# Optimization experiments

Hardware: AMD Instinct MI355X
Metric: run time of the kernel (lower is better)

## Reference

```python
import jax, jax.numpy as jnp
import numpy as np

RATIO, NH, NG, KS, RF, UP = 4, 2, 2, 3, 11.0, 2


def _cln(t, g, b):
    # channel-wise LayerNorm on NCHW (LayerNormProxy), eps=1e-5
    mu = t.mean(axis=1, keepdims=True)
    var = ((t - mu) ** 2).mean(axis=1, keepdims=True)
    return (t - mu) * jax.lax.rsqrt(var + 1e-5) * g[None, :, None, None] + b[None, :, None, None]


def _resize_ac(img, oH, oW):
    # bilinear resize, align_corners=True (F.interpolate)
    H, W = img.shape[-2], img.shape[-1]
    ys = jnp.arange(oH, dtype=img.dtype) * ((H - 1) / (oH - 1))
    y0 = jnp.clip(jnp.floor(ys), 0, H - 2).astype(jnp.int32)
    wy = ys - y0.astype(img.dtype)
    xs = jnp.arange(oW, dtype=img.dtype) * ((W - 1) / (oW - 1))
    x0 = jnp.clip(jnp.floor(xs), 0, W - 2).astype(jnp.int32)
    wx = xs - x0.astype(img.dtype)
    t = img[..., y0, :] * (1.0 - wy)[:, None] + img[..., y0 + 1, :] * wy[:, None]
    return t[..., x0] * (1.0 - wx) + t[..., x0 + 1] * wx


def _grid_sample(img, iy, ix):
    # bilinear grid_sample, padding_mode='zeros', align_corners=True
    # img [Bg,Cx,H,W]; iy,ix [Bg,N] unnormalized input-pixel coords
    H, W = img.shape[-2], img.shape[-1]
    def one(im, yy, xx):
        y0f, x0f = jnp.floor(yy), jnp.floor(xx)
        wy, wx = yy - y0f, xx - x0f
        y0, x0 = y0f.astype(jnp.int32), x0f.astype(jnp.int32)
        def gat(yi, xi):
            valid = ((yi >= 0) & (yi < H) & (xi >= 0) & (xi < W)).astype(im.dtype)
            return im[:, jnp.clip(yi, 0, H - 1), jnp.clip(xi, 0, W - 1)] * valid[None]
        return (gat(y0, x0) * ((1 - wy) * (1 - wx))[None]
                + gat(y0, x0 + 1) * ((1 - wy) * wx)[None]
                + gat(y0 + 1, x0) * (wy * (1 - wx))[None]
                + gat(y0 + 1, x0 + 1) * (wy * wx)[None])
    return jax.vmap(one)(img, iy, ix)


def _conv2d(x, w, groups=1):
    return jax.lax.conv_general_dilated(x, w, (1, 1), 'SAME', feature_group_count=groups,
                                        dimension_numbers=('NCHW', 'OIHW', 'NCHW'))


def _forward(x, ln_g, ln_b, Wq, Wk, dw_w, off_ln_g, off_ln_b, off_w, off_b, rpb):
    B, C, H, W = x.shape
    hidden = C // RATIO
    gc = hidden // NG
    c2 = hidden // NH          # attn_dim per head
    oH, oW = int(H * UP), int(W * UP)
    N1, n = oH * oW, KS * KS
    scale = c2 ** -0.5
    v = x
    xn = _cln(x, ln_g, ln_b)
    q = jnp.einsum('oc,bchw->bohw', Wq, xn)
    k = jnp.einsum('oc,bchw->bohw', Wk, xn)
    q = _resize_ac(q, oH, oW)                        # [B,hidden,oH,oW]
    # offset prediction
    q_off = q.reshape(B * NG, gc, oH, oW)
    t = _conv2d(q_off, dw_w, groups=gc)
    t = _cln(t, off_ln_g, off_ln_b)
    t = jax.nn.gelu(t, approximate=False)
    pred = _conv2d(t, off_w) + off_b[None, :, None, None]  # [Bg,2*ks^2,oH,oW]
    pad = (KS - 1) // 2
    rng = jnp.arange(-pad, pad + 1, dtype=x.dtype)
    base = jnp.stack(jnp.meshgrid(rng, rng, indexing='ij'), axis=-1)  # [KS,KS,2] (y,x)
    off = jnp.tanh(pred).reshape(B * NG, KS, KS, 2, oH, oW) * RF + base[None, :, :, :, None, None]
    py = off[:, :, :, 0] + jnp.arange(oH, dtype=x.dtype)[None, None, None, :, None]
    px = off[:, :, :, 1] + jnp.arange(oW, dtype=x.dtype)[None, None, None, None, :]
    # normalize over (oH-1,oW-1) then denormalize onto (H-1,W-1) input grid (align_corners)
    iy = (py * ((H - 1) / (oH - 1))).reshape(B * NG, -1)
    ix = (px * ((W - 1) / (oW - 1))).reshape(B * NG, -1)
    kg = k.reshape(B * NG, hidden // NG, H, W)
    vg = v.reshape(B * NG, C // NG, H, W)
    kf = _grid_sample(kg, iy, ix).reshape(B, NG, hidden // NG, n, oH, oW)
    vf = _grid_sample(vg, iy, ix).reshape(B, NG, C // NG, n, oH, oW)
    # -> [B, N1, n, g*c] -> [B, nh, N1, n, c]
    kf = kf.transpose(0, 4, 5, 3, 1, 2).reshape(B, N1, n, NH, hidden // NH).transpose(0, 3, 1, 2, 4)
    vf = vf.transpose(0, 4, 5, 3, 1, 2).reshape(B, N1, n, NH, C // NH).transpose(0, 3, 1, 2, 4)
    kf = kf + rpb                                     # relative position bias on K
    qh = q.reshape(B, NH, c2, N1).transpose(0, 1, 3, 2) * scale  # [B,nh,N1,c2]
    attn = jax.nn.softmax(jnp.einsum('bhnc,bhnkc->bhnk', qh, kf), axis=-1)
    out = jnp.einsum('bhnk,bhnkc->bhnc', attn, vf)    # [B,nh,N1,C/nh]
    return out.transpose(0, 1, 3, 2).reshape(B, C, oH, oW)


def setup_inputs() -> dict:
    key = jax.random.key(0)
    ks = jax.random.split(key, 8)
    B, C, H, W = 2, 256, 48, 48
    hidden = C // RATIO
    gc = hidden // NG
    c2 = hidden // NH
    f32 = jnp.float32
    return {
        'x': jax.random.normal(ks[0], (B, C, H, W), f32),
        'ln_g': jnp.ones((C,), f32),
        'ln_b': jnp.zeros((C,), f32),
        'Wq': jax.random.normal(ks[1], (hidden, C), f32) * 0.05,
        'Wk': jax.random.normal(ks[2], (hidden, C), f32) * 0.05,
        'dw_w': jax.random.normal(ks[3], (gc, 1, 3, 3), f32) * 0.1,
        'off_ln_g': jnp.ones((gc,), f32),
        'off_ln_b': jnp.zeros((gc,), f32),
        'off_w': jax.random.normal(ks[4], (2 * KS * KS, gc, 3, 3), f32) * 0.02,
        'off_b': jnp.zeros((2 * KS * KS,), f32),
        'rpb': jax.random.normal(ks[5], (1, NH, 1, KS * KS, c2), f32) * 0.02,
    }


def reference(x, ln_g, ln_b, Wq, Wk, dw_w, off_ln_g, off_ln_b, off_w, off_b, rpb):
    return _forward(x, ln_g, ln_b, Wq, Wk, dw_w, off_ln_g, off_ln_b, off_w, off_b, rpb)
```

## Files before the change

kernel.cpp:

```cpp
#include <hip/hip_runtime.h>
#include <hip/hip_fp16.h>
#include <cstdint>
#include <cmath>

#define NB 2
#define NC 256
#define HW 2304
#define HID 64
#define OH 96
#define OW 96
#define N1 9216
#define SCALE_ATTN 0.17677669529663689f
#define RESZ ((float)(47.0/95.0))

__device__ __host__ inline int ocb8(int w) { return w < 2 ? 3 * w : 6 + 2 * (w - 2); }
__device__ __host__ inline int cnt8(int w) { return w < 2 ? 3 : 2; }

__global__ void kA_prep(const float* __restrict__ x, const float* __restrict__ Wq,
                        const float* __restrict__ Wk, const float* __restrict__ off_w,
                        const float* __restrict__ dw_w, const float* __restrict__ off_b,
                        __half* __restrict__ v_nhwc, float* __restrict__ WT4,
                        float* __restrict__ dwT, float* __restrict__ wg2,
                        float* __restrict__ bsg2) {
    int blk = blockIdx.x;
    if (blk < 1152) {
        int pt = blk % 72;
        int t2 = blk / 72;
        int ct = t2 & 3;
        int bg = t2 >> 2;
        int b = bg >> 1, g = bg & 1;
        __shared__ float tile[32][33];
        int tx = threadIdx.x & 31, row = threadIdx.x >> 5;
#pragma unroll
        for (int r = 0; r < 4; r++) {
            int c = ct * 32 + row + r * 8;
            tile[row + r * 8][tx] = x[((size_t)(b * 256 + g * 128 + c)) * HW + pt * 32 + tx];
        }
        __syncthreads();
#pragma unroll
        for (int r = 0; r < 4; r++) {
            int p = pt * 32 + row + r * 8;
            v_nhwc[((size_t)bg * HW + p) * 128 + ct * 32 + tx] =
                __float2half(tile[tx][row + r * 8]);
        }
    } else {
        int idx = (blk - 1152) * 256 + threadIdx.x;
        if (idx < 32768) {
            int c = idx >> 7, t = idx & 127;
            float v = (t < 64) ? Wq[t * 256 + c] : Wk[(t - 64) * 256 + c];
            WT4[(((size_t)(c >> 2) * 128) + t) * 4 + (c & 3)] = v;
        } else if (idx < 32768 + 288) {
            int i = idx - 32768;
            int wi = i >> 5, c = i & 31;
            dwT[i] = dw_w[c * 9 + wi];
        } else if (idx < 32768 + 288 + 8 * 288 * 3) {
            int i = idx - (32768 + 288);
            int w = i / 864, r = i - w * 864;
            int kk = r / 3, j = r - kk * 3;
            wg2[i] = (j < cnt8(w)) ? off_w[(ocb8(w) + j) * 288 + kk] : 0.f;
        } else if (idx < 32768 + 288 + 8 * 288 * 3 + 24) {
            int i = idx - (32768 + 288 + 8 * 288 * 3);
            int w = i / 3, j = i - w * 3;
            bsg2[i] = (j < cnt8(w)) ? off_b[ocb8(w) + j] : 0.f;
        }
    }
}

__global__ __launch_bounds__(512) void k1_ln_qk(const __half* __restrict__ v_nhwc,
                         const float* __restrict__ ln_g, const float* __restrict__ ln_b,
                         const float* __restrict__ WT4,
                         float* __restrict__ q_pix, __half* __restrict__ k_nhwc) {
    int blk = blockIdx.x;
    int tid = threadIdx.x;
    int wv = tid >> 6, lane = tid & 63;
    __shared__ float xs[8][256];
    {
        int pix = blk * 8 + wv;
        int b = pix / HW, p = pix - b * HW;
        int c0 = lane * 2;
        __half2 h0 = *(const __half2*)(v_nhwc + (((size_t)(b * 2 + 0) * HW) + p) * 128 + c0);
        __half2 h1 = *(const __half2*)(v_nhwc + (((size_t)(b * 2 + 1) * HW) + p) * 128 + c0);
        float2 u0 = __half22float2(h0);
        float2 u1 = __half22float2(h1);
        float s = u0.x + u0.y + u1.x + u1.y;
#pragma unroll
        for (int off = 1; off < 64; off <<= 1) s += __shfl_xor(s, off);
        float mu = s * (1.f / 256.f);
        float d0 = u0.x - mu, d1 = u0.y - mu, d2 = u1.x - mu, d3 = u1.y - mu;
        float q = d0 * d0 + d1 * d1 + d2 * d2 + d3 * d3;
#pragma unroll
        for (int off = 1; off < 64; off <<= 1) q += __shfl_xor(q, off);
        float rs = rsqrtf(q * (1.f / 256.f) + 1e-5f);
        float2 w0, w1;
        w0.x = d0 * rs * ln_g[c0] + ln_b[c0];
        w0.y = d1 * rs * ln_g[c0 + 1] + ln_b[c0 + 1];
        w1.x = d2 * rs * ln_g[128 + c0] + ln_b[128 + c0];
        w1.y = d3 * rs * ln_g[129 + c0] + ln_b[129 + c0];
        *(float2*)&xs[wv][c0] = w0;
        *(float2*)&xs[wv][128 + c0] = w1;
    }
    __syncthreads();
    int o = tid & 127, ph = tid >> 7;
    float a0 = 0.f, a1 = 0.f;
    const float4* wp = (const float4*)WT4 + o;
    const float4* xa = (const float4*)xs[ph * 2];
    const float4* xb4 = (const float4*)xs[ph * 2 + 1];
#pragma unroll 8
    for (int c4 = 0; c4 < 64; c4++) {
        float4 w = wp[(size_t)c4 * 128];
        float4 p0 = xa[c4], p1 = xb4[c4];
        a0 += w.x * p0.x + w.y * p0.y + w.z * p0.z + w.w * p0.w;
        a1 += w.x * p1.x + w.y * p1.y + w.z * p1.z + w.w * p1.w;
    }
#pragma unroll
    for (int k = 0; k < 2; k++) {
        int pix = blk * 8 + ph * 2 + k;
        int b = pix / HW, p = pix - b * HW;
        float a = k ? a1 : a0;
        if (o < 64) {
            q_pix[(((size_t)b * HW) + p) * 64 + o] = a;
        } else {
            int t = o - 64, g = t >> 5, c32 = t & 31;
            k_nhwc[(((size_t)(b * 2 + g) * HW) + p) * 32 + c32] = __float2half(a);
        }
    }
}

__global__ __launch_bounds__(256) void k3_t(const float* __restrict__ q_pix,
                                            const float* __restrict__ dwT,
                                            const float* __restrict__ og,
                                            const float* __restrict__ ob,
                                            __half* __restrict__ tbuf_h,
                                            float* __restrict__ qr) {
    int gid = blockIdx.x * 256 + threadIdx.x;
    int c = gid & 31;
    int p2 = gid >> 5;
    int bg = p2 / N1, p = p2 - bg * N1;
    int b = bg >> 1, g = bg & 1;
    int oy = p / OW, ox = p - oy * OW;
    const float* qb = q_pix + ((size_t)b * HW) * 64 + g * 32 + c;
    float acc = 0.f;
    float qcen = 0.f;
#pragma unroll
    for (int dy = -1; dy <= 1; dy++) {
        int yy = oy + dy;
        if ((unsigned)yy >= (unsigned)OH) continue;
        float ysf = yy * RESZ;
        int y0 = min((int)ysf, 46);
        float wy = ysf - (float)y0;
#pragma unroll
        for (int dx = -1; dx <= 1; dx++) {
            int xx = ox + dx;
            if ((unsigned)xx >= (unsigned)OW) continue;
            float xsf = xx * RESZ;
            int x0 = min((int)xsf, 46);
            float wx = xsf - (float)x0;
            int i00 = (y0 * 48 + x0) * 64;
            float q00 = qb[i00], q01 = qb[i00 + 64];
            float q10 = qb[i00 + 48 * 64], q11 = qb[i00 + 49 * 64];
            float qv = (q00 * (1.f - wy) + q10 * wy) * (1.f - wx)
                     + (q01 * (1.f - wy) + q11 * wy) * wx;
            acc += qv * dwT[((dy + 1) * 3 + dx + 1) * 32 + c];
            if (dy == 0 && dx == 0) qcen = qv;
        }
    }
    float s = acc;
#pragma unroll
    for (int off = 1; off < 32; off <<= 1) s += __shfl_xor(s, off);
    float mu = s * (1.f / 32.f);
    float d = acc - mu;
    float v = d * d;
#pragma unroll
    for (int off = 1; off < 32; off <<= 1) v += __shfl_xor(v, off);
    float rsv = rsqrtf(v * (1.f / 32.f) + 1e-5f);
    float t = d * rsv * og[c] + ob[c];
    float ge = 0.5f * t * (1.f + erff(t * 0.70710678118654752f));
    tbuf_h[(size_t)p2 * 32 + c] = __float2half(ge);
    qr[((size_t)b * N1 + p) * 64 + g * 32 + c] = qcen;
}

__global__ __launch_bounds__(512) void k4_pred(const __half* __restrict__ tbuf_h,
                                               const float* __restrict__ wg2,
                                               const float* __restrict__ bsg2,
                                               float* __restrict__ pred) {
    int blk = blockIdx.x;
    int bg = blk / 144, tile = blk - bg * 144;
    int ty0 = (tile / 12) * 8, tx0 = (tile % 12) * 8;
    int tid = threadIdx.x;
    __shared__ float ts[100 * 33];

    const __half* tb = tbuf_h + (size_t)bg * N1 * 32;
    for (int item = tid; item < 400; item += 512) {
        int pt = item >> 2, qg = item & 3;
        int hy = ty0 + pt / 10 - 1;
        int hx = tx0 + pt % 10 - 1;
        float4 raw = make_float4(0.f, 0.f, 0.f, 0.f);
        if ((unsigned)hy < (unsigned)OH && (unsigned)hx < (unsigned)OW)
            raw = *(const float4*)(tb + ((size_t)(hy * OW + hx)) * 32 + qg * 8);
        const __half2* h2 = (const __half2*)&raw;
        int base = pt * 33 + qg * 8;
#pragma unroll
        for (int i = 0; i < 4; i++) {
            float2 f = __half22float2(h2[i]);
            ts[base + i * 2] = f.x;
            ts[base + i * 2 + 1] = f.y;
        }
    }
    __syncthreads();

    int w = __builtin_amdgcn_readfirstlane(tid >> 6);
    int lane = tid & 63;
    int y = lane >> 3, x = lane & 7;
    int ocb = ocb8(w), cnt = cnt8(w);
    float acc[3];
#pragma unroll
    for (int j = 0; j < 3; j++) acc[j] = bsg2[w * 3 + j];
    const float* tsb = &ts[(y * 10 + x) * 33];
    const float* wgp = wg2 + (size_t)w * 864;
    const int kof[9] = {0, 33, 66, 330, 363, 396, 660, 693, 726};
    for (int ic = 0; ic < 32; ic++) {
#pragma unroll
        for (int k = 0; k < 9; k++) {
            float tv = tsb[kof[k] + ic];
            const float* wr = wgp + (ic * 9 + k) * 3;
#pragma unroll
            for (int j = 0; j < 3; j++) acc[j] += tv * wr[j];
        }
    }
    int p = (ty0 + y) * OW + tx0 + x;
    float* pp = pred + ((size_t)bg * N1 + p) * 18 + ocb;
#pragma unroll
    for (int j = 0; j < 3; j++)
        if (j < cnt) pp[j] = acc[j];
}

__global__ __launch_bounds__(256) void k5_attn(const float* __restrict__ pred,
                                               const float* __restrict__ qr,
                                               const __half* __restrict__ k_nhwc,
                                               const __half* __restrict__ v_nhwc,
                                               const float* __restrict__ rpb,
                                               float* __restrict__ out) {
    int tid = threadIdx.x;
    int wv = __builtin_amdgcn_readfirstlane(tid >> 6);
    int lane = tid & 63;
    int gp = blockIdx.x * 8;
    int bg = gp / N1, p0 = gp % N1;
    int b = bg >> 1, g = bg & 1;
    int pw = p0 + wv * 2;
    int oy = pw / OW, ox0 = pw % OW;

    __shared__ float4 wts[4][2][9];
    __shared__ int4   cof[4][2][9];
    __shared__ float  outb[4][2][128];

    if (lane < 18) {
        int px = lane / 9, j = lane % 9;
        int p = pw + px;
        int ky = j / 3, kx = j % 3;
        const float* pp = pred + ((size_t)bg * N1 + p) * 18;
        float pr0 = pp[j * 2];
        float pr1 = pp[j * 2 + 1];
        float th0 = 1.f - 2.f * __builtin_amdgcn_rcpf(__expf(2.f * pr0) + 1.f);
        float th1 = 1.f - 2.f * __builtin_amdgcn_rcpf(__expf(2.f * pr1) + 1.f);
        float py  = th0 * 11.0f + (float)(ky - 1) + (float)oy;
        float pxc = th1 * 11.0f + (float)(kx - 1) + (float)(ox0 + px);
        float iy = py * RESZ, ix = pxc * RESZ;
        float y0f = floorf(iy), x0f = floorf(ix);
        float wy = iy - y0f, wx = ix - x0f;
        int y0 = (int)y0f, x0 = (int)x0f;
        bool vy0 = (unsigned)y0 < 48u, vy1 = (unsigned)(y0 + 1) < 48u;
        bool vx0 = (unsigned)x0 < 48u, vx1 = (unsigned)(x0 + 1) < 48u;
        int y0c = min(max(y0, 0), 47), y1c = min(max(y0 + 1, 0), 47);
        int x0c = min(max(x0, 0), 47), x1c = min(max(x0 + 1, 0), 47);
        float4 w;
        w.x = (vy0 && vx0) ? (1.f - wy) * (1.f - wx) : 0.f;
        w.y = (vy0 && vx1) ? (1.f - wy) * wx : 0.f;
        w.z = (vy1 && vx0) ? wy * (1.f - wx) : 0.f;
        w.w = (vy1 && vx1) ? wy * wx : 0.f;
        wts[wv][px][j] = w;
        cof[wv][px][j] = make_int4(y0c * 48 + x0c, y0c * 48 + x1c,
                                   y1c * 48 + x0c, y1c * 48 + x1c);
    }
    __syncthreads();

    int c2 = lane & 15, jg = lane >> 4;
    const __half* kb = k_nhwc + (size_t)bg * HW * 32 + 2 * c2;
    const float* rb = rpb + (size_t)g * 288;
    const __half* vb = v_nhwc + (size_t)bg * HW * 128 + c2 * 8;

    float2 rv[3];
#pragma unroll
    for (int jj = 0; jj < 3; jj++) {
        int j = jj * 4 + jg;
        rv[jj] = (j < 9) ? *(const float2*)(rb + j * 32 + 2 * c2) : make_float2(0.f, 0.f);
    }

    const float* qrb = qr + ((size_t)b * N1 + pw) * 64 + g * 32 + 2 * c2;
    float2 qv[2];
    {
        float2 t0 = *(const float2*)qrb;
        float2 t1 = *(const float2*)(qrb + 64);
        qv[0] = make_float2(t0.x * SCALE_ATTN, t0.y * SCALE_ATTN);
        qv[1] = make_float2(t1.x * SCALE_ATTN, t1.y * SCALE_ATTN);
    }

    float s[2][3];
#pragma unroll
    for (int px = 0; px < 2; px++) {
#pragma unroll
        for (int jj = 0; jj < 3; jj++) {
            int j = jj * 4 + jg;
            float partial = 0.f;
            if (j < 9) {
                float4 w = wts[wv][px][j];
                int4 co = cof[wv][px][j];
                float2 k0 = __half22float2(*(const __half2*)(kb + (size_t)co.x * 32));
                float2 k1 = __half22float2(*(const __half2*)(kb + (size_t)co.y * 32));
                float2 k2 = __half22float2(*(const __half2*)(kb + (size_t)co.z * 32));
                float2 k3 = __half22float2(*(const __half2*)(kb + (size_t)co.w * 32));
                float kvx = w.x * k0.x + w.y * k1.x + w.z * k2.x + w.w * k3.x;
                float kvy = w.x * k0.y + w.y * k1.y + w.z * k2.y + w.w * k3.y;
                partial = qv[px].x * (kvx + rv[jj].x) + qv[px].y * (kvy + rv[jj].y);
            }
#pragma unroll
            for (int off = 1; off < 16; off <<= 1) partial += __shfl_xor(partial, off);
            s[px][jj] = (j < 9) ? partial : -1e30f;
        }
    }

    float pj[2][3];
#pragma unroll
    for (int px = 0; px < 2; px++) {
        float m = fmaxf(fmaxf(s[px][0], s[px][1]), s[px][2]);
        m = fmaxf(m, __shfl_xor(m, 16));
        m = fmaxf(m, __shfl_xor(m, 32));
        float e0 = __expf(s[px][0] - m);
        float e1 = __expf(s[px][1] - m);
        float e2 = __expf(s[px][2] - m);
        float sum = e0 + e1 + e2;
        sum += __shfl_xor(sum, 16);
        sum += __shfl_xor(sum, 32);
        float inv = __builtin_amdgcn_rcpf(sum);
        pj[px][0] = e0 * inv; pj[px][1] = e1 * inv; pj[px][2] = e2 * inv;
    }

    __half2 acc[2][4];
#pragma unroll
    for (int px = 0; px < 2; px++)
#pragma unroll
        for (int q = 0; q < 4; q++) acc[px][q] = __float2half2_rn(0.f);

#pragma unroll
    for (int px = 0; px < 2; px++) {
#pragma unroll
        for (int jj = 0; jj < 3; jj++) {
            int j = jj * 4 + jg;
            if (j < 9) {
                float p = pj[px][jj];
                float4 w = wts[wv][px][j];
                int4 co = cof[wv][px][j];
                float4 r0 = *(const float4*)(vb + (size_t)co.x * 128);
                float4 r1 = *(const float4*)(vb + (size_t)co.y * 128);
                float4 r2 = *(const float4*)(vb + (size_t)co.z * 128);
                float4 r3 = *(const float4*)(vb + (size_t)co.w * 128);
                const __half2* A0 = (const __half2*)&r0;
                const __half2* A1 = (const __half2*)&r1;
                const __half2* A2 = (const __half2*)&r2;
                const __half2* A3 = (const __half2*)&r3;
                __half2 f0 = __float2half2_rn(w.x * p);
                __half2 f1 = __float2half2_rn(w.y * p);
                __half2 f2 = __float2half2_rn(w.z * p);
                __half2 f3 = __float2half2_rn(w.w * p);
#pragma unroll
                for (int q = 0; q < 4; q++) {
                    acc[px][q] = __hfma2(f0, A0[q], acc[px][q]);
                    acc[px][q] = __hfma2(f1, A1[q], acc[px][q]);
                    acc[px][q] = __hfma2(f2, A2[q], acc[px][q]);
                    acc[px][q] = __hfma2(f3, A3[q], acc[px][q]);
                }
            }
        }
    }

#pragma unroll
    for (int px = 0; px < 2; px++) {
        float f[8];
#pragma unroll
        for (int q = 0; q < 4; q++) {
            float2 t = __half22float2(acc[px][q]);
            f[2 * q] = t.x; f[2 * q + 1] = t.y;
        }
#pragma unroll
        for (int i = 0; i < 8; i++) {
            f[i] += __shfl_xor(f[i], 16);
            f[i] += __shfl_xor(f[i], 32);
        }
        if (lane < 16) {
            *(float4*)&outb[wv][px][c2 * 8]     = make_float4(f[0], f[1], f[2], f[3]);
            *(float4*)&outb[wv][px][c2 * 8 + 4] = make_float4(f[4], f[5], f[6], f[7]);
        }
    }
    __syncthreads();

    {
        int ch = tid & 127, qh = tid >> 7;
        float* op = out + ((size_t)b * NC + g * 128 + ch) * N1 + p0 + qh * 4;
        float4 v4 = make_float4(outb[qh * 2][0][ch], outb[qh * 2][1][ch],
                                outb[qh * 2 + 1][0][ch], outb[qh * 2 + 1][1][ch]);
        *(float4*)op = v4;
    }
}

extern "C" void kernel_launch(void* const* d_in, const int* in_sizes, int n_in,
                              void* d_out, int out_size, void* d_ws, size_t ws_size,
                              hipStream_t stream) {
    const float* x      = (const float*)d_in[0];
    const float* ln_g   = (const float*)d_in[1];
    const float* ln_b   = (const float*)d_in[2];
    const float* Wq     = (const float*)d_in[3];
    const float* Wk     = (const float*)d_in[4];
    const float* dw_w   = (const float*)d_in[5];
    const float* off_g  = (const float*)d_in[6];
    const float* off_bt = (const float*)d_in[7];
    const float* off_w  = (const float*)d_in[8];
    const float* off_b  = (const float*)d_in[9];
    const float* rpb    = (const float*)d_in[10];
    float* out = (float*)d_out;

    float* ws = (float*)d_ws;
    float* WT4    = ws;
    float* q_pix  = WT4 + 32768;
    float* pred   = q_pix + 294912;
    float* dwT    = pred + 663552;
    float* wg2    = dwT + 288;
    float* bsg2   = wg2 + 6912;
    __half* v_nhwc = (__half*)(bsg2 + 24);
    __half* k_nhwc = v_nhwc + 1179648;
    __half* tbuf_h = k_nhwc + 294912;
    float* qr      = (float*)(tbuf_h + 1179648);

    kA_prep<<<1309, 256, 0, stream>>>(x, Wq, Wk, off_w, dw_w, off_b,
                                      v_nhwc, WT4, dwT, wg2, bsg2);
    k1_ln_qk<<<576, 512, 0, stream>>>(v_nhwc, ln_g, ln_b, WT4, q_pix, k_nhwc);
    k3_t<<<4608, 256, 0, stream>>>(q_pix, dwT, off_g, off_bt, tbuf_h, qr);
    k4_pred<<<576, 512, 0, stream>>>(tbuf_h, wg2, bsg2, pred);
    k5_attn<<<4608, 256, 0, stream>>>(pred, qr, k_nhwc, v_nhwc, rpb, out);
}
```

Measured before the change: 155.6 us.

## Fuse offset-branch dwconv/LN/GELU into offset-prediction conv kernel via shared-memory tiles

Merges the upsample+depthwise conv+LayerNorm+GELU kernel into the 3x3 offset-prediction conv kernel. Each 8x8 output tile first computes a 12x12 halo of bilinearly resized q values in shared memory, then the 10x10 t halo, then the conv. This removes the fp16 tbuf round trip through global memory and one launch. In exchange it recomputes t on halos (about 1.56x) and the resize values on a wider halo, and it runs with fewer blocks and more shared memory per block.

```diff
diff --git a/kernel.cpp b/kernel.cpp
--- a/kernel.cpp
+++ b/kernel.cpp
@@ -126,84 +126,85 @@
     }
 }
 
-__global__ __launch_bounds__(256) void k3_t(const float* __restrict__ q_pix,
-                                            const float* __restrict__ dwT,
-                                            const float* __restrict__ og,
-                                            const float* __restrict__ ob,
-                                            __half* __restrict__ tbuf_h,
-                                            float* __restrict__ qr) {
-    int gid = blockIdx.x * 256 + threadIdx.x;
-    int c = gid & 31;
-    int p2 = gid >> 5;
-    int bg = p2 / N1, p = p2 - bg * N1;
-    int b = bg >> 1, g = bg & 1;
-    int oy = p / OW, ox = p - oy * OW;
-    const float* qb = q_pix + ((size_t)b * HW) * 64 + g * 32 + c;
-    float acc = 0.f;
-    float qcen = 0.f;
-#pragma unroll
-    for (int dy = -1; dy <= 1; dy++) {
-        int yy = oy + dy;
-        if ((unsigned)yy >= (unsigned)OH) continue;
-        float ysf = yy * RESZ;
-        int y0 = min((int)ysf, 46);
-        float wy = ysf - (float)y0;
-#pragma unroll
-        for (int dx = -1; dx <= 1; dx++) {
-            int xx = ox + dx;
-            if ((unsigned)xx >= (unsigned)OW) continue;
-            float xsf = xx * RESZ;
-            int x0 = min((int)xsf, 46);
-            float wx = xsf - (float)x0;
-            int i00 = (y0 * 48 + x0) * 64;
-            float q00 = qb[i00], q01 = qb[i00 + 64];
-            float q10 = qb[i00 + 48 * 64], q11 = qb[i00 + 49 * 64];
-            float qv = (q00 * (1.f - wy) + q10 * wy) * (1.f - wx)
-                     + (q01 * (1.f - wy) + q11 * wy) * wx;
-            acc += qv * dwT[((dy + 1) * 3 + dx + 1) * 32 + c];
-            if (dy == 0 && dx == 0) qcen = qv;
-        }
-    }
-    float s = acc;
-#pragma unroll
-    for (int off = 1; off < 32; off <<= 1) s += __shfl_xor(s, off);
-    float mu = s * (1.f / 32.f);
-    float d = acc - mu;
-    float v = d * d;
-#pragma unroll
-    for (int off = 1; off < 32; off <<= 1) v += __shfl_xor(v, off);
-    float rsv = rsqrtf(v * (1.f / 32.f) + 1e-5f);
-    float t = d * rsv * og[c] + ob[c];
-    float ge = 0.5f * t * (1.f + erff(t * 0.70710678118654752f));
-    tbuf_h[(size_t)p2 * 32 + c] = __float2half(ge);
-    qr[((size_t)b * N1 + p) * 64 + g * 32 + c] = qcen;
-}
-
-__global__ __launch_bounds__(512) void k4_pred(const __half* __restrict__ tbuf_h,
-                                               const float* __restrict__ wg2,
-                                               const float* __restrict__ bsg2,
-                                               float* __restrict__ pred) {
+__global__ __launch_bounds__(512) void k34_t_pred(const float* __restrict__ q_pix,
+                                                  const float* __restrict__ dwT,
+                                                  const float* __restrict__ og,
+                                                  const float* __restrict__ ob,
+                                                  const float* __restrict__ wg2,
+                                                  const float* __restrict__ bsg2,
+                                                  float* __restrict__ qr,
+                                                  float* __restrict__ pred) {
     int blk = blockIdx.x;
     int bg = blk / 144, tile = blk - bg * 144;
     int ty0 = (tile / 12) * 8, tx0 = (tile % 12) * 8;
     int tid = threadIdx.x;
+    int b = bg >> 1, g = bg & 1;
+
+    __shared__ float rq[144 * 32];
     __shared__ float ts[100 * 33];
 
-    const __half* tb = tbuf_h + (size_t)bg * N1 * 32;
-    for (int item = tid; item < 400; item += 512) {
-        int pt = item >> 2, qg = item & 3;
-        int hy = ty0 + pt / 10 - 1;
-        int hx = tx0 + pt % 10 - 1;
-        float4 raw = make_float4(0.f, 0.f, 0.f, 0.f);
-        if ((unsigned)hy < (unsigned)OH && (unsigned)hx < (unsigned)OW)
-            raw = *(const float4*)(tb + ((size_t)(hy * OW + hx)) * 32 + qg * 8);
-        const __half2* h2 = (const __half2*)&raw;
-        int base = pt * 33 + qg * 8;
-#pragma unroll
-        for (int i = 0; i < 4; i++) {
-            float2 f = __half22float2(h2[i]);
-            ts[base + i * 2] = f.x;
-            ts[base + i * 2 + 1] = f.y;
+    const float* qb = q_pix + (size_t)b * HW * 64 + g * 32;
+
+    for (int item = tid; item < 144 * 32; item += 512) {
+        int pt = item >> 5, c = item & 31;
+        int ry = ty0 + (pt / 12) - 2;
+        int rx = tx0 + (pt % 12) - 2;
+        float val = 0.f;
+        if ((unsigned)ry < 96u && (unsigned)rx < 96u) {
+            float ysf = ry * RESZ;
+            int y0 = min((int)ysf, 46);
+            float wy = ysf - (float)y0;
+            float xsf = rx * RESZ;
+            int x0 = min((int)xsf, 46);
+            float wx = xsf - (float)x0;
+            const float* q0 = qb + (y0 * 48 + x0) * 64 + c;
+            float q00 = q0[0], q01 = q0[64];
+            float q10 = q0[48 * 64], q11 = q0[49 * 64];
+            val = (q00 * (1.f - wy) + q10 * wy) * (1.f - wx)
+                + (q01 * (1.f - wy) + q11 * wy) * wx;
+        }
+        rq[pt * 32 + c] = val;
+    }
+    __syncthreads();
+
+    for (int item = tid; item < 64 * 32; item += 512) {
+        int pt = item >> 5, c = item & 31;
+        int iy = pt >> 3, ix = pt & 7;
+        int p = (ty0 + iy) * OW + tx0 + ix;
+        int rpt = (iy + 2) * 12 + (ix + 2);
+        qr[((size_t)b * N1 + p) * 64 + g * 32 + c] = rq[rpt * 32 + c];
+    }
+
+    {
+        int c = tid & 31, grp = tid >> 5;
+        for (int pass = 0; pass < 7; pass++) {
+            int pt = pass * 16 + grp;
+            if (pt < 100) {
+                int u = pt / 10, v = pt - u * 10;
+                int hy = ty0 + u - 1, hx = tx0 + v - 1;
+                float tval = 0.f;
+                if ((unsigned)hy < 96u && (unsigned)hx < 96u) {
+                    float acc = 0.f;
+#pragma unroll
+                    for (int dy = 0; dy < 3; dy++)
+#pragma unroll
+                        for (int dx = 0; dx < 3; dx++)
+                            acc += rq[((u + dy) * 12 + (v + dx)) * 32 + c]
+                                 * dwT[(dy * 3 + dx) * 32 + c];
+                    float s = acc;
+#pragma unroll
+                    for (int off = 1; off < 32; off <<= 1) s += __shfl_xor(s, off);
+                    float mu = s * (1.f / 32.f);
+                    float d = acc - mu;
+                    float vv = d * d;
+#pragma unroll
+                    for (int off = 1; off < 32; off <<= 1) vv += __shfl_xor(vv, off);
+                    float rsv = rsqrtf(vv * (1.f / 32.f) + 1e-5f);
+                    float t = d * rsv * og[c] + ob[c];
+                    tval = 0.5f * t * (1.f + erff(t * 0.70710678118654752f));
+                }
+                ts[pt * 33 + c] = tval;
+            }
         }
     }
     __syncthreads();
@@ -436,13 +437,12 @@
     float* bsg2   = wg2 + 6912;
     __half* v_nhwc = (__half*)(bsg2 + 24);
     __half* k_nhwc = v_nhwc + 1179648;
-    __half* tbuf_h = k_nhwc + 294912;
-    float* qr      = (float*)(tbuf_h + 1179648);
+    float* qr      = (float*)(k_nhwc + 294912);
 
     kA_prep<<<1309, 256, 0, stream>>>(x, Wq, Wk, off_w, dw_w, off_b,
                                       v_nhwc, WT4, dwT, wg2, bsg2);
     k1_ln_qk<<<576, 512, 0, stream>>>(v_nhwc, ln_g, ln_b, WT4, q_pix, k_nhwc);
-    k3_t<<<4608, 256, 0, stream>>>(q_pix, dwT, off_g, off_bt, tbuf_h, qr);
-    k4_pred<<<576, 512, 0, stream>>>(tbuf_h, wg2, bsg2, pred);
+    k34_t_pred<<<576, 512, 0, stream>>>(q_pix, dwT, off_g, off_bt, wg2, bsg2,
+                                        qr, pred);
     k5_attn<<<4608, 256, 0, stream>>>(pred, qr, k_nhwc, v_nhwc, rpb, out);
 }
```

New measurement: 154.6 us, median of 2. Within noise of the previous version (-0.6%).
